# Optimization experiments

Hardware: AMD Instinct MI355X
Metric: run time of the kernel (lower is better)

## Reference

```python
import jax, jax.numpy as jnp
import numpy as np

N = 64    # state dim n
K = 8     # mixture components
H = 1024  # fhat hidden
B = 65536
LOG2PI = float(np.log(2.0 * np.pi))

def setup_inputs() -> dict:
    key = jax.random.key(0)
    ks = jax.random.split(key, 8)
    x = jax.random.normal(ks[0], (B, N), jnp.float32)
    y = jax.random.normal(ks[1], (B, 1, N), jnp.float32)
    W1 = jax.random.normal(ks[2], (N, H), jnp.float32) / np.sqrt(N)
    b1 = jnp.zeros((H,), jnp.float32)
    W2 = jax.random.normal(ks[3], (H, 2 * K * N), jnp.float32) / np.sqrt(H)
    b2 = jnp.zeros((2 * K * N,), jnp.float32)
    Wp1 = jax.random.normal(ks[4], (N, N), jnp.float32) / np.sqrt(N)
    bp1 = jnp.zeros((N,), jnp.float32)
    Wp2 = jax.random.normal(ks[5], (N, K), jnp.float32) / np.sqrt(N)
    bp2 = jnp.zeros((K,), jnp.float32)
    return {"x": x, "y": y, "W1": W1, "b1": b1, "W2": W2, "b2": b2,
            "Wp1": Wp1, "bp1": bp1, "Wp2": Wp2, "bp2": bp2}

def _mdn_view(t):
    # torch.stack(t.split(n, dim=1)).view(-1, k, n): raw reshape of [k,B,n] -> [B,k,n]
    return jnp.stack(jnp.split(t, K, axis=1)).reshape(-1, K, N)

def reference(x, y, W1, b1, W2, b2, Wp1, bp1, Wp2, bp2):
    # fhat: Linear -> ELU -> Linear
    fhatx = jax.nn.elu(x @ W1 + b1) @ W2 + b2          # [B, 2*K*N]
    mu_raw, var_raw = jnp.split(fhatx, 2, axis=-1)     # each [B, K*N]
    mu = _mdn_view(mu_raw)                             # [B, K, N]
    var = jnp.maximum(jnp.exp(_mdn_view(var_raw)), 1e-8)
    # pi network: log probs of OneHotCategorical
    logits = jax.nn.elu(x @ Wp1 + bp1) @ Wp2 + bp2     # [B, K]
    log_pi = jax.nn.log_softmax(logits, axis=-1)
    # diagonal-covariance MVN log_prob (closed form, O(n))
    d = y - mu                                         # [B, K, N]
    logp_y = -0.5 * (jnp.sum(d * d / var + jnp.log(var), axis=-1) + N * LOG2PI)
    loss = jax.scipy.special.logsumexp(log_pi + logp_y, axis=-1)  # [B]
    return -jnp.mean(loss)
```

## Files before the change

kernel.cpp:

```cpp
#include <hip/hip_runtime.h>
#include <math.h>

typedef __attribute__((ext_vector_type(8))) _Float16 half8;
typedef __attribute__((ext_vector_type(4))) _Float16 half4;
typedef __attribute__((ext_vector_type(4))) float f32x4;

#define B_TOT 65536
#define LOG2PI_F 1.8378770664093453f
#define HALF_N_LOG2PI (0.5f * 64.0f * LOG2PI_F)
#define LOG_1EM8 (-18.420680743952367f)

#define WS_W2S  0
#define WS_W1P  (2u*1024*1024)
#define WS_LPS  (4u*1024*1024)
#define WS_PART (6u*1024*1024)
#define WS_HP   (8u*1024*1024)

typedef __attribute__((address_space(3))) unsigned int lds_u32;
typedef const __attribute__((address_space(1))) unsigned int glb_u32;

__device__ __forceinline__ void gload16(const void* g, void* l) {
    __builtin_amdgcn_global_load_lds((glb_u32*)g, (lds_u32*)l, 16, 0, 0);
}

__device__ __forceinline__ float eluf(float v) {
    return v > 0.0f ? v : expm1f(v);
}

__global__ __launch_bounds__(256)
void pack_w1(const float* __restrict__ src, _Float16* __restrict__ dst)
{
    __shared__ float ts[64][65];
    const int t = threadIdx.x;
    const int n0 = blockIdx.y * 64;
    {
        int r = t >> 2, c4 = t & 3;
        for (int i = 0; i < 4; ++i) {
            int cc = i * 4 + c4;
            float4 v = *(const float4*)&src[(size_t)r * 1024 + n0 + cc * 4];
            ts[r][cc*4+0] = v.x; ts[r][cc*4+1] = v.y;
            ts[r][cc*4+2] = v.z; ts[r][cc*4+3] = v.w;
        }
    }
    __syncthreads();
    {
        int n = t >> 2;
        for (int i = 0; i < 4; ++i) {
            int k = (i * 4 + (t & 3)) * 4;
            half4 h;
            h.x = (_Float16)ts[k+0][n];
            h.y = (_Float16)ts[k+1][n];
            h.z = (_Float16)ts[k+2][n];
            h.w = (_Float16)ts[k+3][n];
            size_t off = (size_t)(k >> 5) * 32768 + (size_t)(n0 + n) * 32 + (k & 31);
            *(half4*)&dst[off] = h;
        }
    }
}

__global__ __launch_bounds__(256)
void pack_w2s(const float* __restrict__ src, _Float16* __restrict__ dst)
{
    __shared__ float ts[64][65];
    const int t = threadIdx.x;
    const int k0 = blockIdx.x * 64, n0 = blockIdx.y * 64;
    {
        int r = t >> 2, c4 = t & 3;
        for (int i = 0; i < 4; ++i) {
            int cc = i * 4 + c4;
            float4 v = *(const float4*)&src[(size_t)(k0 + r) * 1024 + n0 + cc * 4];
            ts[r][cc*4+0] = v.x; ts[r][cc*4+1] = v.y;
            ts[r][cc*4+2] = v.z; ts[r][cc*4+3] = v.w;
        }
    }
    __syncthreads();
    {
        int n = t >> 2;
        int ng = n0 + n;
        for (int i = 0; i < 4; ++i) {
            int kl = (i * 4 + (t & 3)) * 4;
            int k = k0 + kl;
            half4 h;
            h.x = (_Float16)ts[kl+0][n];
            h.y = (_Float16)ts[kl+1][n];
            h.z = (_Float16)ts[kl+2][n];
            h.w = (_Float16)ts[kl+3][n];
            int kk = k & 31;
            int slot = ((kk >> 3) ^ ((ng >> 1) & 3));
            size_t off = (size_t)(k >> 5) * 32768 + (size_t)ng * 32 + (slot << 3) + (kk & 7);
            *(half4*)&dst[off] = h;
        }
    }
}

__global__ __launch_bounds__(512)
void k1_h(const float* __restrict__ x, const _Float16* __restrict__ W1P,
          const float* __restrict__ b1, _Float16* __restrict__ hp)
{
    __shared__ __align__(16) _Float16 xs[32 * 64];
    const int t = threadIdx.x, q = blockIdx.x;
    const int w = t >> 6, l = t & 63, g = l >> 4, l15 = l & 15;

    {
        const float4* x4 = (const float4*)x;
        int r = t >> 4, c = t & 15;
        float4 v = x4[(size_t)(q * 32 + r) * 16 + c];
        float vv[4] = {v.x, v.y, v.z, v.w};
        #pragma unroll
        for (int i = 0; i < 4; ++i) {
            int col = c * 4 + i;
            xs[r * 64 + (col ^ ((r & 7) << 3))] = (_Float16)vv[i];
        }
    }
    __syncthreads();

    f32x4 acc[8][2];
    const float4* b1_4 = (const float4*)b1;
    #pragma unroll
    for (int nf = 0; nf < 8; ++nf) {
        float4 bv = b1_4[(w * 128 + nf * 16 + 4 * g) >> 2];
        acc[nf][0] = (f32x4){bv.x, bv.y, bv.z, bv.w};
        acc[nf][1] = acc[nf][0];
    }
    #pragma unroll
    for (int k0 = 0; k0 < 64; k0 += 32) {
        half8 bx[2];
        #pragma unroll
        for (int rf = 0; rf < 2; ++rf) {
            int row = rf * 16 + l15;
            bx[rf] = *(const half8*)&xs[row * 64 + ((k0 + 8 * g) ^ ((row & 7) << 3))];
        }
        #pragma unroll
        for (int nf = 0; nf < 8; ++nf) {
            size_t off = (size_t)(k0 >> 5) * 32768 + (size_t)(w * 128 + nf * 16 + l15) * 32 + 8 * g;
            half8 aw = *(const half8*)&W1P[off];
            #pragma unroll
            for (int rf = 0; rf < 2; ++rf)
                acc[nf][rf] = __builtin_amdgcn_mfma_f32_16x16x32_f16(aw, bx[rf], acc[nf][rf], 0, 0, 0);
        }
    }
    #pragma unroll
    for (int nf = 0; nf < 8; ++nf) {
        int kt = w * 4 + (nf >> 1);
        int kkhi = (nf & 1) * 2 + (g >> 1);
        int kklo = 4 * (g & 1);
        #pragma unroll
        for (int rf = 0; rf < 2; ++rf) {
            int grow = q * 32 + rf * 16 + l15;
            int slot = kkhi ^ ((grow >> 1) & 3);
            half4 h4;
            h4.x = (_Float16)eluf(acc[nf][rf][0]);
            h4.y = (_Float16)eluf(acc[nf][rf][1]);
            h4.z = (_Float16)eluf(acc[nf][rf][2]);
            h4.w = (_Float16)eluf(acc[nf][rf][3]);
            *(half4*)&hp[(size_t)kt * 2097152 + (size_t)grow * 32 + slot * 8 + kklo] = h4;
        }
    }
}

__global__ __launch_bounds__(512)
void k2_gemm2(const _Float16* __restrict__ hp, const _Float16* __restrict__ W2S,
              const float* __restrict__ b2, const float* __restrict__ y,
              float* __restrict__ lps)
{
    __shared__ __align__(16) _Float16 Ab[2][4096];
    __shared__ __align__(16) _Float16 Bb[2][8192];
    __shared__ float lpp[128][2][2];

    const int t = threadIdx.x;
    const int bid = blockIdx.x;
    const int logical = (bid & 7) * 256 + (bid >> 3);
    const int RT = logical >> 2;
    const int j  = logical & 3;
    const int w = t >> 6, l = t & 63, g = l >> 4, l15 = l & 15;
    const int wr = w >> 2, wc = w & 3;

    int bn[4];
    bn[0] = (wc >> 1) * 64 + (wc & 1) * 32 + l15;
    bn[1] = bn[0] + 16;
    bn[2] = bn[0] + 128;
    bn[3] = bn[1] + 128;

    f32x4 acc[4][4];
    #pragma unroll
    for (int fc = 0; fc < 4; ++fc) {
        int colg = (fc < 2) ? (j * 128 + bn[fc]) : (512 + j * 128 + bn[fc] - 128);
        float bv = b2[colg];
        #pragma unroll
        for (int fr = 0; fr < 4; ++fr) acc[fr][fc] = (f32x4){bv, bv, bv, bv};
    }

    const char* hpb  = (const char*)hp;
    const char* w2sb = (const char*)W2S;
    const int lane16 = l * 16;

    {
        size_t ga = ((size_t)0 * 65536 + (size_t)RT * 128) * 64 + w * 1024 + lane16;
        gload16(hpb + ga, (char*)&Ab[0][0] + w * 1024);
        size_t gb0 = ((size_t)0 * 1024 + j * 128) * 64 + w * 1024 + lane16;
        gload16(w2sb + gb0, (char*)&Bb[0][0] + w * 1024);
        size_t gb1 = ((size_t)0 * 1024 + 512 + j * 128) * 64 + w * 1024 + lane16;
        gload16(w2sb + gb1, (char*)&Bb[0][0] + 8192 + w * 1024);
    }
    __syncthreads();

    for (int kt = 0; kt < 32; ++kt) {
        int cur = kt & 1;
        if (kt < 31) {
            int nx = cur ^ 1;
            size_t ga = ((size_t)(kt + 1) * 65536 + (size_t)RT * 128) * 64 + w * 1024 + lane16;
            gload16(hpb + ga, (char*)&Ab[nx][0] + w * 1024);
            size_t gb0 = ((size_t)(kt + 1) * 1024 + j * 128) * 64 + w * 1024 + lane16;
            gload16(w2sb + gb0, (char*)&Bb[nx][0] + w * 1024);
            size_t gb1 = ((size_t)(kt + 1) * 1024 + 512 + j * 128) * 64 + w * 1024 + lane16;
            gload16(w2sb + gb1, (char*)&Bb[nx][0] + 8192 + w * 1024);
        }
        half8 aF[4], bF[4];
        #pragma unroll
        for (int fr = 0; fr < 4; ++fr) {
            int r = wr * 64 + fr * 16 + l15;
            aF[fr] = *(const half8*)((const char*)&Ab[cur][0] + r * 64 + ((g ^ ((r >> 1) & 3)) << 4));
        }
        #pragma unroll
        for (int fc = 0; fc < 4; ++fc) {
            int n = bn[fc];
            bF[fc] = *(const half8*)((const char*)&Bb[cur][0] + n * 64 + ((g ^ ((n >> 1) & 3)) << 4));
        }
        #pragma unroll
        for (int fc = 0; fc < 4; ++fc)
            #pragma unroll
            for (int fr = 0; fr < 4; ++fr)
                acc[fr][fc] = __builtin_amdgcn_mfma_f32_16x16x32_f16(aF[fr], bF[fc], acc[fr][fc], 0, 0, 0);
        __syncthreads();
    }

    const int jj = j * 2 + (wc >> 1);
    float s[4][4];
    #pragma unroll
    for (int fr = 0; fr < 4; ++fr)
        #pragma unroll
        for (int rg = 0; rg < 4; ++rg) s[fr][rg] = 0.0f;

    #pragma unroll
    for (int fc = 0; fc < 2; ++fc) {
        int n = (wc & 1) * 32 + fc * 16 + l15;
        #pragma unroll
        for (int fr = 0; fr < 4; ++fr)
            #pragma unroll
            for (int rg = 0; rg < 4; ++rg) {
                int grow = RT * 128 + wr * 64 + fr * 16 + 4 * g + rg;
                int bp = (grow >> 3) + jj * 8192;
                float yv = y[(size_t)bp * 64 + n];
                float mu = acc[fr][fc][rg];
                float vr = acc[fr][fc + 2][rg];
                float vre = fmaxf(vr, LOG_1EM8);
                float iv = (vr >= LOG_1EM8) ? expf(-vr) : 1e8f;
                float d = yv - mu;
                s[fr][rg] += fmaf(d * d, iv, vre);
            }
    }
    #pragma unroll
    for (int fr = 0; fr < 4; ++fr)
        #pragma unroll
        for (int rg = 0; rg < 4; ++rg) {
            float v = s[fr][rg];
            v += __shfl_xor(v, 1); v += __shfl_xor(v, 2);
            v += __shfl_xor(v, 4); v += __shfl_xor(v, 8);
            s[fr][rg] = v;
        }
    if (l15 == 0) {
        #pragma unroll
        for (int fr = 0; fr < 4; ++fr)
            #pragma unroll
            for (int rg = 0; rg < 4; ++rg)
                lpp[wr * 64 + fr * 16 + 4 * g + rg][wc >> 1][wc & 1] = s[fr][rg];
    }
    __syncthreads();
    if (t < 256) {
        int row_l = t >> 1, m = t & 1;
        float lp = -0.5f * (lpp[row_l][m][0] + lpp[row_l][m][1]) - HALF_N_LOG2PI;
        int grow = RT * 128 + row_l;
        int bp = (grow >> 3) + (j * 2 + m) * 8192;
        lps[(size_t)bp * 8 + (grow & 7)] = lp;
    }
}

__global__ __launch_bounds__(256)
void k3_pi(const float* __restrict__ x, const float* __restrict__ Wp1,
           const float* __restrict__ bp1, const float* __restrict__ Wp2,
           const float* __restrict__ bp2, const float* __restrict__ lps,
           float* __restrict__ partials)
{
    __shared__ float xsl[256][65];
    __shared__ float w1s[64][65];
    __shared__ float w2s[64][8];
    __shared__ float wsum[4];
    const int t = threadIdx.x;
    const int b0 = blockIdx.x * 256;

    {
        const float4* x4 = (const float4*)x;
        for (int i = 0; i < 16; ++i) {
            int idx = t + i * 256;
            int r = idx >> 4, c = idx & 15;
            float4 v = x4[(size_t)(b0 + r) * 16 + c];
            xsl[r][c*4+0] = v.x; xsl[r][c*4+1] = v.y;
            xsl[r][c*4+2] = v.z; xsl[r][c*4+3] = v.w;
        }
        for (int i = 0; i < 16; ++i) {
            int idx = t + i * 256;
            int r = idx >> 6, c = idx & 63;
            w1s[r][c] = Wp1[r * 64 + c];
        }
        ((float*)w2s)[t] = Wp2[t];
        ((float*)w2s)[t + 256] = Wp2[t + 256];
    }
    __syncthreads();

    float hid[64];
    #pragma unroll
    for (int c = 0; c < 64; ++c) hid[c] = bp1[c];
    for (int n = 0; n < 64; ++n) {
        float xv = xsl[t][n];
        #pragma unroll
        for (int c = 0; c < 64; ++c) hid[c] = fmaf(xv, w1s[n][c], hid[c]);
    }
    float lg[8];
    #pragma unroll
    for (int k = 0; k < 8; ++k) lg[k] = bp2[k];
    #pragma unroll
    for (int c = 0; c < 64; ++c) {
        float e = eluf(hid[c]);
        #pragma unroll
        for (int k = 0; k < 8; ++k) lg[k] = fmaf(e, w2s[c][k], lg[k]);
    }
    float4 lpa = *(const float4*)&lps[(size_t)(b0 + t) * 8];
    float4 lpb = *(const float4*)&lps[(size_t)(b0 + t) * 8 + 4];
    float lp[8] = {lpa.x, lpa.y, lpa.z, lpa.w, lpb.x, lpb.y, lpb.z, lpb.w};

    float m1 = lg[0];
    #pragma unroll
    for (int k = 1; k < 8; ++k) m1 = fmaxf(m1, lg[k]);
    float den = 0.0f;
    #pragma unroll
    for (int k = 0; k < 8; ++k) den += expf(lg[k] - m1);
    float lden = logf(den);

    float v0 = lg[0] - m1 - lden + lp[0];
    float m2 = v0;
    float vv[8]; vv[0] = v0;
    #pragma unroll
    for (int k = 1; k < 8; ++k) {
        vv[k] = lg[k] - m1 - lden + lp[k];
        m2 = fmaxf(m2, vv[k]);
    }
    float s2 = 0.0f;
    #pragma unroll
    for (int k = 0; k < 8; ++k) s2 += expf(vv[k] - m2);
    float loss = m2 + logf(s2);

    float ssum = loss;
    ssum += __shfl_xor(ssum, 1);  ssum += __shfl_xor(ssum, 2);
    ssum += __shfl_xor(ssum, 4);  ssum += __shfl_xor(ssum, 8);
    ssum += __shfl_xor(ssum, 16); ssum += __shfl_xor(ssum, 32);
    if ((t & 63) == 0) wsum[t >> 6] = ssum;
    __syncthreads();
    if (t == 0) partials[blockIdx.x] = wsum[0] + wsum[1] + wsum[2] + wsum[3];
}

__global__ void k4_reduce(const float* __restrict__ partials, float* __restrict__ out)
{
    __shared__ double red[256];
    int t = threadIdx.x;
    red[t] = (double)partials[t];
    __syncthreads();
    for (int s = 128; s > 0; s >>= 1) {
        if (t < s) red[t] += red[t + s];
        __syncthreads();
    }
    if (t == 0) out[0] = (float)(-red[0] / (double)B_TOT);
}

extern "C" void kernel_launch(void* const* d_in, const int* in_sizes, int n_in,
                              void* d_out, int out_size, void* d_ws, size_t ws_size,
                              hipStream_t stream)
{
    const float* x   = (const float*)d_in[0];
    const float* y   = (const float*)d_in[1];
    const float* W1  = (const float*)d_in[2];
    const float* b1  = (const float*)d_in[3];
    const float* W2  = (const float*)d_in[4];
    const float* b2  = (const float*)d_in[5];
    const float* Wp1 = (const float*)d_in[6];
    const float* bp1 = (const float*)d_in[7];
    const float* Wp2 = (const float*)d_in[8];
    const float* bp2 = (const float*)d_in[9];

    char* ws = (char*)d_ws;
    _Float16* W2S = (_Float16*)(ws + WS_W2S);
    _Float16* W1P = (_Float16*)(ws + WS_W1P);
    float* lps      = (float*)(ws + WS_LPS);
    float* partials = (float*)(ws + WS_PART);
    _Float16* hp    = (_Float16*)(ws + WS_HP);

    pack_w2s<<<dim3(16, 16), 256, 0, stream>>>(W2, W2S);
    pack_w1<<<dim3(1, 16), 256, 0, stream>>>(W1, W1P);
    k1_h<<<2048, 512, 0, stream>>>(x, W1P, b1, hp);
    k2_gemm2<<<2048, 512, 0, stream>>>(hp, W2S, b2, y, lps);
    k3_pi<<<256, 256, 0, stream>>>(x, Wp1, bp1, Wp2, bp2, lps, partials);
    k4_reduce<<<1, 256, 0, stream>>>(partials, (float*)d_out);
}
```

Measured before the change: 248.6 us.

## Triple-buffer GEMM2 LDS staging with prefetch distance two and single barrier

```diff
diff --git a/kernel.cpp b/kernel.cpp
--- a/kernel.cpp
+++ b/kernel.cpp
@@ -163,8 +163,8 @@
               const float* __restrict__ b2, const float* __restrict__ y,
               float* __restrict__ lps)
 {
-    __shared__ __align__(16) _Float16 Ab[2][4096];
-    __shared__ __align__(16) _Float16 Bb[2][8192];
+    __shared__ __align__(16) _Float16 Ab[3][4096];
+    __shared__ __align__(16) _Float16 Bb[3][8192];
     __shared__ float lpp[128][2][2];
 
     const int t = threadIdx.x;
@@ -194,45 +194,55 @@
     const char* w2sb = (const char*)W2S;
     const int lane16 = l * 16;
 
-    {
-        size_t ga = ((size_t)0 * 65536 + (size_t)RT * 128) * 64 + w * 1024 + lane16;
-        gload16(hpb + ga, (char*)&Ab[0][0] + w * 1024);
-        size_t gb0 = ((size_t)0 * 1024 + j * 128) * 64 + w * 1024 + lane16;
-        gload16(w2sb + gb0, (char*)&Bb[0][0] + w * 1024);
-        size_t gb1 = ((size_t)0 * 1024 + 512 + j * 128) * 64 + w * 1024 + lane16;
-        gload16(w2sb + gb1, (char*)&Bb[0][0] + 8192 + w * 1024);
-    }
-    __syncthreads();
-
+    #define STAGE(KT, B)                                                                     \
+    {                                                                                        \
+        size_t ga = ((size_t)(KT) * 65536 + (size_t)RT * 128) * 64 + w * 1024 + lane16;      \
+        gload16(hpb + ga, (char*)&Ab[(B)][0] + w * 1024);                                    \
+        size_t gb0 = ((size_t)(KT) * 1024 + j * 128) * 64 + w * 1024 + lane16;               \
+        gload16(w2sb + gb0, (char*)&Bb[(B)][0] + w * 1024);                                  \
+        size_t gb1 = ((size_t)(KT) * 1024 + 512 + j * 128) * 64 + w * 1024 + lane16;         \
+        gload16(w2sb + gb1, (char*)&Bb[(B)][0] + 8192 + w * 1024);                           \
+    }
+
+    STAGE(0, 0);
+    STAGE(1, 1);
+
+    int cur = 0;
     for (int kt = 0; kt < 32; ++kt) {
-        int cur = kt & 1;
         if (kt < 31) {
-            int nx = cur ^ 1;
-            size_t ga = ((size_t)(kt + 1) * 65536 + (size_t)RT * 128) * 64 + w * 1024 + lane16;
-            gload16(hpb + ga, (char*)&Ab[nx][0] + w * 1024);
-            size_t gb0 = ((size_t)(kt + 1) * 1024 + j * 128) * 64 + w * 1024 + lane16;
-            gload16(w2sb + gb0, (char*)&Bb[nx][0] + w * 1024);
-            size_t gb1 = ((size_t)(kt + 1) * 1024 + 512 + j * 128) * 64 + w * 1024 + lane16;
-            gload16(w2sb + gb1, (char*)&Bb[nx][0] + 8192 + w * 1024);
+            asm volatile("s_waitcnt vmcnt(3)" ::: "memory");
+        } else {
+            asm volatile("s_waitcnt vmcnt(0)" ::: "memory");
+        }
+        __builtin_amdgcn_s_barrier();
+        __builtin_amdgcn_sched_barrier(0);
+        if (kt + 2 < 32) {
+            int nb = cur + 2; if (nb >= 3) nb -= 3;
+            STAGE(kt + 2, nb);
         }
         half8 aF[4], bF[4];
+        const char* Abc = (const char*)&Ab[cur][0];
+        const char* Bbc = (const char*)&Bb[cur][0];
         #pragma unroll
         for (int fr = 0; fr < 4; ++fr) {
             int r = wr * 64 + fr * 16 + l15;
-            aF[fr] = *(const half8*)((const char*)&Ab[cur][0] + r * 64 + ((g ^ ((r >> 1) & 3)) << 4));
+            aF[fr] = *(const half8*)(Abc + r * 64 + ((g ^ ((r >> 1) & 3)) << 4));
         }
         #pragma unroll
         for (int fc = 0; fc < 4; ++fc) {
             int n = bn[fc];
-            bF[fc] = *(const half8*)((const char*)&Bb[cur][0] + n * 64 + ((g ^ ((n >> 1) & 3)) << 4));
-        }
+            bF[fc] = *(const half8*)(Bbc + n * 64 + ((g ^ ((n >> 1) & 3)) << 4));
+        }
+        __builtin_amdgcn_s_setprio(1);
         #pragma unroll
         for (int fc = 0; fc < 4; ++fc)
             #pragma unroll
             for (int fr = 0; fr < 4; ++fr)
                 acc[fr][fc] = __builtin_amdgcn_mfma_f32_16x16x32_f16(aF[fr], bF[fc], acc[fr][fc], 0, 0, 0);
-        __syncthreads();
-    }
+        __builtin_amdgcn_s_setprio(0);
+        cur = (cur == 2) ? 0 : cur + 1;
+    }
+    #undef STAGE
 
     const int jj = j * 2 + (wc >> 1);
     float s[4][4];
```

Result: slower. 336.1 us (+35.2%).
